# Kernel optimization log

Hardware: AMD Instinct MI355X
Metric: run time of the kernel (lower is better)

Reference implementation:

```python
import jax, jax.numpy as jnp
import numpy as np

HEAD_NUM = 8
KEY_DIM = 16
EMBEDDING_DIM = 128
LOGIT_CLIPPING = 10.0

B, G, P, E = 512, 100, 100, 128


def setup_inputs() -> dict:
    key = jax.random.key(0)
    ks = jax.random.split(key, 9)
    return {
        "input1": jax.random.normal(ks[0], (B, 1, E), jnp.float32),
        "input2": jax.random.normal(ks[1], (B, G, E), jnp.float32),
        "remaining_loaded": jax.random.uniform(ks[2], (B, G, 1), jnp.float32),
        "ninf_mask": jnp.zeros((B, G, P), jnp.float32),
        "encoded_nodes": jax.random.normal(ks[3], (B, P, E), jnp.float32),
        "Wq": jax.random.normal(ks[4], (2 * E + 1, HEAD_NUM * KEY_DIM), jnp.float32) * 0.05,
        "Wk": jax.random.normal(ks[5], (E, HEAD_NUM * KEY_DIM), jnp.float32) * 0.05,
        "Wv": jax.random.normal(ks[6], (E, HEAD_NUM * KEY_DIM), jnp.float32) * 0.05,
        "Wc": jax.random.normal(ks[7], (HEAD_NUM * KEY_DIM, E), jnp.float32) * 0.05,
        "bc": jnp.zeros((E,), jnp.float32),
    }


def _heads(x):  # [B, N, H*K] -> [B, H, N, K]
    b, n, _ = x.shape
    return x.reshape(b, n, HEAD_NUM, KEY_DIM).transpose(0, 2, 1, 3)


def reference(input1, input2, remaining_loaded, ninf_mask, encoded_nodes, Wq, Wk, Wv, Wc, bc):
    group_s = input2.shape[1]
    # reset(): precompute keys/values from encoded nodes
    k = _heads(encoded_nodes @ Wk)  # [B,H,P,K]
    v = _heads(encoded_nodes @ Wv)  # [B,H,P,K]
    # forward()
    input_cat = jnp.concatenate(
        [jnp.broadcast_to(input1, (input1.shape[0], group_s, input1.shape[2])),
         input2, remaining_loaded], axis=2)  # [B,G,2E+1]
    q = _heads(input_cat @ Wq)  # [B,H,G,K]
    # multi-head attention with additive ninf mask
    score = jnp.einsum("bhgk,bhpk->bhgp", q, k) / np.sqrt(KEY_DIM).astype(np.float32)
    score = score + ninf_mask[:, None, :, :]
    weights = jax.nn.softmax(score, axis=3)
    out = jnp.einsum("bhgp,bhpk->bhgk", weights, v)  # [B,H,G,K]
    out_concat = out.transpose(0, 2, 1, 3).reshape(out.shape[0], group_s, HEAD_NUM * KEY_DIM)
    mh_atten_out = out_concat @ Wc + bc  # [B,G,E]
    # single-head pointer scoring with tanh clipping
    score2 = jnp.einsum("bge,bpe->bgp", mh_atten_out, encoded_nodes) / np.sqrt(EMBEDDING_DIM).astype(np.float32)
    score_masked = LOGIT_CLIPPING * jnp.tanh(score2) + ninf_mask
    probs = jax.nn.softmax(score_masked, axis=2)
    return probs
```

## Files before the change

kernel.cpp:

```cpp
#include <hip/hip_runtime.h>

#define NB 512
#define NG 100
#define NP 100
#define NE 128
#define NH 8

typedef __attribute__((ext_vector_type(8))) short short8;
typedef __attribute__((ext_vector_type(4))) short short4v;
typedef __attribute__((ext_vector_type(4))) float f32x4;

__device__ __forceinline__ short f2bf(float f) {
    union { float f; unsigned u; } v; v.f = f;
    unsigned r = v.u + 0x7FFFu + ((v.u >> 16) & 1u);
    return (short)(r >> 16);
}

__device__ __forceinline__ f32x4 mfma16(short4v a, short4v b, f32x4 c) {
#if __has_builtin(__builtin_amdgcn_mfma_f32_16x16x16_bf16)
    return __builtin_amdgcn_mfma_f32_16x16x16_bf16(a, b, c, 0, 0, 0);
#elif __has_builtin(__builtin_amdgcn_mfma_f32_16x16x16bf16_1k)
    return __builtin_amdgcn_mfma_f32_16x16x16bf16_1k(a, b, c, 0, 0, 0);
#else
    f32x4 d;
    asm volatile("v_mfma_f32_16x16x16_bf16 %0, %1, %2, %3"
                 : "=&v"(d) : "v"(a), "v"(b), "v"(c));
    return d;
#endif
}

__device__ __forceinline__ f32x4 mfma32(short8 a, short8 b, f32x4 c) {
    return __builtin_amdgcn_mfma_f32_16x16x32_bf16(a, b, c, 0, 0, 0);
}

__global__ void prep_kernel(const float* __restrict__ Wq, const float* __restrict__ Wk,
                            const float* __restrict__ Wv, const float* __restrict__ Wc,
                            short* __restrict__ WqT2, short* __restrict__ WkT,
                            short* __restrict__ WvT, short* __restrict__ WqT1,
                            short* __restrict__ WcB)
{
    int idx = blockIdx.x * 256 + threadIdx.x;
    int mat = idx >> 14;
    int e   = idx & 16383;
    int k = e >> 7, n = e & 127;
    if (mat == 0)      WqT2[n * 128 + k] = f2bf(Wq[(128 + k) * 128 + n]);
    else if (mat == 1) WkT [n * 128 + k] = f2bf(Wk[k * 128 + n]);
    else if (mat == 2) WvT [n * 128 + k] = f2bf(Wv[k * 128 + n]);
    else if (mat == 3)
        WcB[(((n >> 4) << 3) + (k >> 4)) * 256 + ((n & 15) << 4) + (k & 15)] = f2bf(Wc[k * 128 + n]);
    else               WqT1[n * 128 + k] = f2bf(Wq[k * 128 + n]);
}

__global__ __launch_bounds__(448, 2)
void fused_kernel(const float* __restrict__ input1, const float* __restrict__ input2,
                  const float* __restrict__ rem, const float* __restrict__ mask,
                  const float* __restrict__ enc, const float* __restrict__ Wq,
                  const float* __restrict__ bc,
                  const short* __restrict__ WqT2, const short* __restrict__ WkT,
                  const short* __restrict__ WvT, const short* __restrict__ WqT1,
                  const short* __restrict__ WcB, float* __restrict__ out)
{
    __shared__ short sKV[2 * 56 * 256];
    short* sK = sKV;
    short* sV = sKV + 56 * 256;

    const int b    = blockIdx.x;
    const int tid  = threadIdx.x;
    const int wave = tid >> 6, lane = tid & 63;
    const int l16  = lane & 15, lh = lane >> 4;
    const int g    = wave * 16 + l16;
    const bool gok = (g < NG);
    const float NINF = -__builtin_inff();

    short4v qb[8];
    {
        const float* xrow = input2 + ((size_t)b * NG + g) * NE;
        const float* i1   = input1 + (size_t)b * NE;
        short8 xb[4], yb[4];
        #pragma unroll
        for (int ks = 0; ks < 4; ++ks) {
            f32x4 v0 = {0.f,0.f,0.f,0.f}, v1 = {0.f,0.f,0.f,0.f};
            if (gok) {
                v0 = *(const f32x4*)(xrow + ks * 32 + lh * 8);
                v1 = *(const f32x4*)(xrow + ks * 32 + lh * 8 + 4);
            }
            xb[ks] = (short8){ f2bf(v0[0]), f2bf(v0[1]), f2bf(v0[2]), f2bf(v0[3]),
                               f2bf(v1[0]), f2bf(v1[1]), f2bf(v1[2]), f2bf(v1[3]) };
            f32x4 u0 = *(const f32x4*)(i1 + ks * 32 + lh * 8);
            f32x4 u1 = *(const f32x4*)(i1 + ks * 32 + lh * 8 + 4);
            yb[ks] = (short8){ f2bf(u0[0]), f2bf(u0[1]), f2bf(u0[2]), f2bf(u0[3]),
                               f2bf(u1[0]), f2bf(u1[1]), f2bf(u1[2]), f2bf(u1[3]) };
        }
        float remv = gok ? rem[(size_t)b * NG + g] : 0.f;
        #pragma unroll
        for (int nt = 0; nt < 8; ++nt) {
            f32x4 acc0 = {0.f, 0.f, 0.f, 0.f}, acc1 = {0.f, 0.f, 0.f, 0.f};
            #pragma unroll
            for (int ks = 0; ks < 4; ++ks) {
                short8 a2 = *(const short8*)(WqT2 + (nt * 16 + l16) * NE + ks * 32 + lh * 8);
                acc0 = mfma32(a2, xb[ks], acc0);
                short8 a1 = *(const short8*)(WqT1 + (nt * 16 + l16) * NE + ks * 32 + lh * 8);
                acc1 = mfma32(a1, yb[ks], acc1);
            }
            f32x4 wlv = *(const f32x4*)(Wq + 256 * NE + nt * 16 + lh * 4);
            short4v q;
            #pragma unroll
            for (int r = 0; r < 4; ++r)
                q[r] = f2bf(0.25f * (acc0[r] + acc1[r] + remv * wlv[r]));
            qb[nt] = q;
        }
    }

    {
        int row = wave * 16 + l16;
        int rc  = row < NP ? row : NP - 1;
        const float* er = enc + ((size_t)b * NP + rc) * NE;
        short8 eb[4];
        #pragma unroll
        for (int ks = 0; ks < 4; ++ks) {
            f32x4 u0 = *(const f32x4*)(er + ks * 32 + lh * 8);
            f32x4 u1 = *(const f32x4*)(er + ks * 32 + lh * 8 + 4);
            eb[ks] = (short8){ f2bf(u0[0]), f2bf(u0[1]), f2bf(u0[2]), f2bf(u0[3]),
                               f2bf(u1[0]), f2bf(u1[1]), f2bf(u1[2]), f2bf(u1[3]) };
        }
        #pragma unroll
        for (int h = 0; h < NH; ++h) {
            f32x4 a0 = {0.f,0.f,0.f,0.f}, a1 = {0.f,0.f,0.f,0.f};
            #pragma unroll
            for (int ks = 0; ks < 4; ++ks) {
                short8 w = *(const short8*)(WkT + (h * 16 + l16) * NE + ks * 32 + lh * 8);
                if (ks < 2) a0 = mfma32(eb[ks], w, a0);
                else        a1 = mfma32(eb[ks], w, a1);
            }
            f32x4 acc = a0 + a1;
            int base = (h * 7 + wave) * 256;
            #pragma unroll
            for (int r = 0; r < 4; ++r)
                sK[base + (lh * 4 + r) * 16 + l16] = f2bf(acc[r]);
        }
        #pragma unroll
        for (int kb = 0; kb < 8; ++kb) {
            f32x4 a0 = {0.f,0.f,0.f,0.f}, a1 = {0.f,0.f,0.f,0.f};
            #pragma unroll
            for (int ks = 0; ks < 4; ++ks) {
                short8 a = *(const short8*)(WvT + (kb * 16 + l16) * NE + ks * 32 + lh * 8);
                if (ks < 2) a0 = mfma32(a, eb[ks], a0);
                else        a1 = mfma32(a, eb[ks], a1);
            }
            f32x4 acc = a0 + a1;
            int base = (kb * 7 + wave) * 256;
            bool pz = (wave == 6) && (l16 >= 4);
            #pragma unroll
            for (int r = 0; r < 4; ++r)
                sV[base + (lh * 4 + r) * 16 + l16] = pz ? (short)0 : f2bf(acc[r]);
        }
    }

    f32x4 mkv[7];
    {
        const float* mrow = mask + ((size_t)b * NG + (gok ? g : 0)) * NP;
        #pragma unroll
        for (int pt = 0; pt < 7; ++pt) {
            bool ld = gok && (pt < 6 || lh == 0);
            mkv[pt] = ld ? *(const f32x4*)(mrow + pt * 16 + lh * 4)
                         : (f32x4){NINF, NINF, NINF, NINF};
        }
    }
    __syncthreads();

    short4v ocb[8];
    #pragma unroll
    for (int h = 0; h < NH; ++h) {
        float vals[7][4];
        #pragma unroll
        for (int pt = 0; pt < 7; ++pt) {
            short4v kf = *(const short4v*)(sK + (h * 7 + pt) * 256 + l16 * 16 + lh * 4);
            f32x4 z = {0.f, 0.f, 0.f, 0.f};
            f32x4 sc = mfma16(kf, qb[h], z);
            #pragma unroll
            for (int r = 0; r < 4; ++r)
                vals[pt][r] = sc[r] + mkv[pt][r];
        }
        float mr0 = vals[0][0], mr1 = vals[0][1], mr2 = vals[0][2], mr3 = vals[0][3];
        #pragma unroll
        for (int pt = 1; pt < 7; ++pt) {
            mr0 = fmaxf(mr0, vals[pt][0]); mr1 = fmaxf(mr1, vals[pt][1]);
            mr2 = fmaxf(mr2, vals[pt][2]); mr3 = fmaxf(mr3, vals[pt][3]);
        }
        float m = fmaxf(fmaxf(mr0, mr1), fmaxf(mr2, mr3));
        m = fmaxf(m, __shfl_xor(m, 16));
        m = fmaxf(m, __shfl_xor(m, 32));
        float s0 = 0.f, s1 = 0.f, s2 = 0.f, s3 = 0.f;
        #pragma unroll
        for (int pt = 0; pt < 7; ++pt) {
            float e0 = __expf(vals[pt][0] - m); vals[pt][0] = e0; s0 += e0;
            float e1 = __expf(vals[pt][1] - m); vals[pt][1] = e1; s1 += e1;
            float e2 = __expf(vals[pt][2] - m); vals[pt][2] = e2; s2 += e2;
            float e3 = __expf(vals[pt][3] - m); vals[pt][3] = e3; s3 += e3;
        }
        float s = (s0 + s1) + (s2 + s3);
        s += __shfl_xor(s, 16);
        s += __shfl_xor(s, 32);
        float inv = 1.f / s;
        f32x4 o0 = {0.f, 0.f, 0.f, 0.f}, o1 = {0.f, 0.f, 0.f, 0.f};
        #pragma unroll
        for (int pt = 0; pt < 7; ++pt) {
            short4v pb = { f2bf(vals[pt][0] * inv), f2bf(vals[pt][1] * inv),
                           f2bf(vals[pt][2] * inv), f2bf(vals[pt][3] * inv) };
            short4v vf = *(const short4v*)(sV + (h * 7 + pt) * 256 + l16 * 16 + lh * 4);
            if (pt & 1) o1 = mfma16(vf, pb, o1);
            else        o0 = mfma16(vf, pb, o0);
        }
        f32x4 o = o0 + o1;
        ocb[h] = (short4v){ f2bf(o[0]), f2bf(o[1]), f2bf(o[2]), f2bf(o[3]) };
    }

    short4v mhb[8];
    #pragma unroll
    for (int nt = 0; nt < 8; ++nt) {
        f32x4 acc0 = {0.f, 0.f, 0.f, 0.f}, acc1 = {0.f, 0.f, 0.f, 0.f};
        #pragma unroll
        for (int kt = 0; kt < 8; ++kt) {
            short4v a = *(const short4v*)(WcB + (nt * 8 + kt) * 256 + l16 * 16 + lh * 4);
            if (kt < 4) acc0 = mfma16(a, ocb[kt], acc0);
            else        acc1 = mfma16(a, ocb[kt], acc1);
        }
        f32x4 acc = acc0 + acc1;
        f32x4 bcv = *(const f32x4*)(bc + nt * 16 + lh * 4);
        mhb[nt] = (short4v){ f2bf((acc[0] + bcv[0]) * 0.08838834764831845f),
                             f2bf((acc[1] + bcv[1]) * 0.08838834764831845f),
                             f2bf((acc[2] + bcv[2]) * 0.08838834764831845f),
                             f2bf((acc[3] + bcv[3]) * 0.08838834764831845f) };
    }

    const float* encb = enc + (size_t)b * NP * NE;
    const float* mrow = mask + ((size_t)b * NG + (gok ? g : 0)) * NP;
    float vals2[7][4];
    #pragma unroll
    for (int pt = 0; pt < 7; ++pt) {
        int prow = pt * 16 + l16;
        const float* erow = encb + (size_t)(prow < NP ? prow : NP - 1) * NE;
        f32x4 a0 = {0.f,0.f,0.f,0.f}, a1 = {0.f,0.f,0.f,0.f};
        #pragma unroll
        for (int kt = 0; kt < 8; ++kt) {
            f32x4 ev = *(const f32x4*)(erow + kt * 16 + lh * 4);
            short4v ef = { f2bf(ev[0]), f2bf(ev[1]), f2bf(ev[2]), f2bf(ev[3]) };
            if (kt < 4) a0 = mfma16(ef, mhb[kt], a0);
            else        a1 = mfma16(ef, mhb[kt], a1);
        }
        f32x4 acc = a0 + a1;
        bool ld = gok && (pt < 6 || lh == 0);
        f32x4 mv = ld ? *(const f32x4*)(mrow + pt * 16 + lh * 4)
                      : (f32x4){NINF, NINF, NINF, NINF};
        #pragma unroll
        for (int r = 0; r < 4; ++r) {
            float x = acc[r];
            float th = 1.f - 2.f / (__expf(2.f * x) + 1.f);
            vals2[pt][r] = 10.f * th + mv[r];
        }
    }
    {
        float mr0 = vals2[0][0], mr1 = vals2[0][1], mr2 = vals2[0][2], mr3 = vals2[0][3];
        #pragma unroll
        for (int pt = 1; pt < 7; ++pt) {
            mr0 = fmaxf(mr0, vals2[pt][0]); mr1 = fmaxf(mr1, vals2[pt][1]);
            mr2 = fmaxf(mr2, vals2[pt][2]); mr3 = fmaxf(mr3, vals2[pt][3]);
        }
        float m = fmaxf(fmaxf(mr0, mr1), fmaxf(mr2, mr3));
        m = fmaxf(m, __shfl_xor(m, 16));
        m = fmaxf(m, __shfl_xor(m, 32));
        float s0 = 0.f, s1 = 0.f, s2 = 0.f, s3 = 0.f;
        #pragma unroll
        for (int pt = 0; pt < 7; ++pt) {
            float e0 = __expf(vals2[pt][0] - m); vals2[pt][0] = e0; s0 += e0;
            float e1 = __expf(vals2[pt][1] - m); vals2[pt][1] = e1; s1 += e1;
            float e2 = __expf(vals2[pt][2] - m); vals2[pt][2] = e2; s2 += e2;
            float e3 = __expf(vals2[pt][3] - m); vals2[pt][3] = e3; s3 += e3;
        }
        float s = (s0 + s1) + (s2 + s3);
        s += __shfl_xor(s, 16);
        s += __shfl_xor(s, 32);
        float inv = 1.f / s;
        float* orow = out + ((size_t)b * NG + g) * NP;
        #pragma unroll
        for (int pt = 0; pt < 7; ++pt) {
            bool st = gok && (pt < 6 || lh == 0);
            if (st) {
                f32x4 ov = { vals2[pt][0] * inv, vals2[pt][1] * inv,
                             vals2[pt][2] * inv, vals2[pt][3] * inv };
                *(f32x4*)(orow + pt * 16 + lh * 4) = ov;
            }
        }
    }
}

extern "C" void kernel_launch(void* const* d_in, const int* in_sizes, int n_in,
                              void* d_out, int out_size, void* d_ws, size_t ws_size,
                              hipStream_t stream)
{
    const float* input1 = (const float*)d_in[0];
    const float* input2 = (const float*)d_in[1];
    const float* rem    = (const float*)d_in[2];
    const float* mask   = (const float*)d_in[3];
    const float* enc    = (const float*)d_in[4];
    const float* Wq     = (const float*)d_in[5];
    const float* Wk     = (const float*)d_in[6];
    const float* Wv     = (const float*)d_in[7];
    const float* Wc     = (const float*)d_in[8];
    const float* bc     = (const float*)d_in[9];

    short* WqT2 = (short*)d_ws;
    short* WkT  = WqT2 + 16384;
    short* WvT  = WkT + 16384;
    short* WqT1 = WvT + 16384;
    short* WcB  = WqT1 + 16384;

    prep_kernel<<<320, 256, 0, stream>>>(Wq, Wk, Wv, Wc, WqT2, WkT, WvT, WqT1, WcB);

    fused_kernel<<<NB, 448, 0, stream>>>(
        input1, input2, rem, mask, enc, Wq, bc,
        WqT2, WkT, WvT, WqT1, WcB, (float*)d_out);
}
```

Measured before the change: 217.2 us.

## Pack two batches per 896-thread block and pad K/V shared tiles

The fused kernel now handles two batch elements per block using 14 waves, with dynamic shared memory. K/V tiles use a padded row stride of 20 shorts to reduce LDS bank conflicts on fragment reads. The prep kernel now has each thread load 8 contiguous floats with vector loads, which cuts its grid from 320 to 40 blocks. Launching 896-thread blocks changes occupancy and register limits and could reduce per-SM concurrency.

```diff
diff --git a/kernel.cpp b/kernel.cpp
--- a/kernel.cpp
+++ b/kernel.cpp
@@ -5,6 +5,11 @@
 #define NP 100
 #define NE 128
 #define NH 8
+
+#define RS 20
+#define TS 320
+#define SUB_SHORTS (2 * 56 * TS)
+#define SMEM_BYTES (2 * SUB_SHORTS * 2)
 
 typedef __attribute__((ext_vector_type(8))) short short8;
 typedef __attribute__((ext_vector_type(4))) short short4v;
@@ -40,18 +45,31 @@
                             short* __restrict__ WcB)
 {
     int idx = blockIdx.x * 256 + threadIdx.x;
-    int mat = idx >> 14;
-    int e   = idx & 16383;
-    int k = e >> 7, n = e & 127;
-    if (mat == 0)      WqT2[n * 128 + k] = f2bf(Wq[(128 + k) * 128 + n]);
-    else if (mat == 1) WkT [n * 128 + k] = f2bf(Wk[k * 128 + n]);
-    else if (mat == 2) WvT [n * 128 + k] = f2bf(Wv[k * 128 + n]);
-    else if (mat == 3)
-        WcB[(((n >> 4) << 3) + (k >> 4)) * 256 + ((n & 15) << 4) + (k & 15)] = f2bf(Wc[k * 128 + n]);
-    else               WqT1[n * 128 + k] = f2bf(Wq[k * 128 + n]);
-}
-
-__global__ __launch_bounds__(448, 2)
+    int mat = idx >> 11;
+    int e   = idx & 2047;
+    int k = e >> 4, n0 = (e & 15) * 8;
+    const float* src;
+    if (mat == 0)      src = Wq + (size_t)(128 + k) * 128 + n0;
+    else if (mat == 1) src = Wk + (size_t)k * 128 + n0;
+    else if (mat == 2) src = Wv + (size_t)k * 128 + n0;
+    else if (mat == 3) src = Wc + (size_t)k * 128 + n0;
+    else               src = Wq + (size_t)k * 128 + n0;
+    f32x4 a = *(const f32x4*)src;
+    f32x4 c = *(const f32x4*)(src + 4);
+    float vv[8] = {a[0], a[1], a[2], a[3], c[0], c[1], c[2], c[3]};
+    #pragma unroll
+    for (int i = 0; i < 8; ++i) {
+        int n = n0 + i;
+        short h = f2bf(vv[i]);
+        if (mat == 0)      WqT2[n * 128 + k] = h;
+        else if (mat == 1) WkT [n * 128 + k] = h;
+        else if (mat == 2) WvT [n * 128 + k] = h;
+        else if (mat == 3) WcB[(((n >> 4) << 3) + (k >> 4)) * 256 + ((n & 15) << 4) + (k & 15)] = h;
+        else               WqT1[n * 128 + k] = h;
+    }
+}
+
+__global__ __launch_bounds__(896, 1)
 void fused_kernel(const float* __restrict__ input1, const float* __restrict__ input2,
                   const float* __restrict__ rem, const float* __restrict__ mask,
                   const float* __restrict__ enc, const float* __restrict__ Wq,
@@ -60,17 +78,20 @@
                   const short* __restrict__ WvT, const short* __restrict__ WqT1,
                   const short* __restrict__ WcB, float* __restrict__ out)
 {
-    __shared__ short sKV[2 * 56 * 256];
-    short* sK = sKV;
-    short* sV = sKV + 56 * 256;
-
-    const int b    = blockIdx.x;
+    extern __shared__ short smem[];
+
     const int tid  = threadIdx.x;
     const int wave = tid >> 6, lane = tid & 63;
+    const int sub  = (wave >= 7) ? 1 : 0;
+    const int wv   = wave - sub * 7;
+    const int b    = blockIdx.x * 2 + sub;
     const int l16  = lane & 15, lh = lane >> 4;
-    const int g    = wave * 16 + l16;
+    const int g    = wv * 16 + l16;
     const bool gok = (g < NG);
     const float NINF = -__builtin_inff();
+
+    short* sK = smem + sub * SUB_SHORTS;
+    short* sV = sK + 56 * TS;
 
     short4v qb[8];
     {
@@ -112,7 +133,7 @@
     }
 
     {
-        int row = wave * 16 + l16;
+        int row = wv * 16 + l16;
         int rc  = row < NP ? row : NP - 1;
         const float* er = enc + ((size_t)b * NP + rc) * NE;
         short8 eb[4];
@@ -133,10 +154,10 @@
                 else        a1 = mfma32(eb[ks], w, a1);
             }
             f32x4 acc = a0 + a1;
-            int base = (h * 7 + wave) * 256;
+            int base = (h * 7 + wv) * TS;
             #pragma unroll
             for (int r = 0; r < 4; ++r)
-                sK[base + (lh * 4 + r) * 16 + l16] = f2bf(acc[r]);
+                sK[base + (lh * 4 + r) * RS + l16] = f2bf(acc[r]);
         }
         #pragma unroll
         for (int kb = 0; kb < 8; ++kb) {
@@ -148,11 +169,11 @@
                 else        a1 = mfma32(a, eb[ks], a1);
             }
             f32x4 acc = a0 + a1;
-            int base = (kb * 7 + wave) * 256;
-            bool pz = (wave == 6) && (l16 >= 4);
+            int base = (kb * 7 + wv) * TS;
+            bool pz = (wv == 6) && (l16 >= 4);
             #pragma unroll
             for (int r = 0; r < 4; ++r)
-                sV[base + (lh * 4 + r) * 16 + l16] = pz ? (short)0 : f2bf(acc[r]);
+                sV[base + (lh * 4 + r) * RS + l16] = pz ? (short)0 : f2bf(acc[r]);
         }
     }
 
@@ -174,7 +195,7 @@
         float vals[7][4];
         #pragma unroll
         for (int pt = 0; pt < 7; ++pt) {
-            short4v kf = *(const short4v*)(sK + (h * 7 + pt) * 256 + l16 * 16 + lh * 4);
+            short4v kf = *(const short4v*)(sK + (h * 7 + pt) * TS + l16 * RS + lh * 4);
             f32x4 z = {0.f, 0.f, 0.f, 0.f};
             f32x4 sc = mfma16(kf, qb[h], z);
             #pragma unroll
@@ -207,7 +228,7 @@
         for (int pt = 0; pt < 7; ++pt) {
             short4v pb = { f2bf(vals[pt][0] * inv), f2bf(vals[pt][1] * inv),
                            f2bf(vals[pt][2] * inv), f2bf(vals[pt][3] * inv) };
-            short4v vf = *(const short4v*)(sV + (h * 7 + pt) * 256 + l16 * 16 + lh * 4);
+            short4v vf = *(const short4v*)(sV + (h * 7 + pt) * TS + l16 * RS + lh * 4);
             if (pt & 1) o1 = mfma16(vf, pb, o1);
             else        o0 = mfma16(vf, pb, o0);
         }
@@ -315,9 +336,11 @@
     short* WqT1 = WvT + 16384;
     short* WcB  = WqT1 + 16384;
 
-    prep_kernel<<<320, 256, 0, stream>>>(Wq, Wk, Wv, Wc, WqT2, WkT, WvT, WqT1, WcB);
-
-    fused_kernel<<<NB, 448, 0, stream>>>(
+    prep_kernel<<<40, 256, 0, stream>>>(Wq, Wk, Wv, Wc, WqT2, WkT, WvT, WqT1, WcB);
+
+    hipFuncSetAttribute((const void*)fused_kernel,
+                        hipFuncAttributeMaxDynamicSharedMemorySize, SMEM_BYTES);
+    fused_kernel<<<NB / 2, 896, SMEM_BYTES, stream>>>(
         input1, input2, rem, mask, enc, Wq, bc,
         WqT2, WkT, WvT, WqT1, WcB, (float*)d_out);
 }
```

Result: slower. 244.4 us (+12.6%).
